# Performance work log

Measured on AMD Instinct MI355X. Metric: run time of the kernel, lower is better.

The kernel has to match this reference:

```python
import jax, jax.numpy as jnp
import numpy as np

NS = 50000   # number of source cells
NT = 50000   # number of target cells
E = 1_600_000  # nnz of neighborhood (avg degree 32)
DIN = 64
DOUT = 64


def setup_inputs() -> dict:
    key = jax.random.key(0)
    ks = jax.random.split(key, 14)
    w_scale = ((2.0 / (DIN + DOUT)) ** 0.5) * 1.414  # xavier_uniform-ish std with gain
    a_scale = (1.0 / (3 * DOUT)) ** 0.5
    nrm = lambda k, s, sc: jax.random.normal(k, s, jnp.float32) * sc
    return {
        "x_source": jax.random.normal(ks[0], (NS, DIN), jnp.float32),
        "x_target": jax.random.normal(ks[1], (NT, DIN), jnp.float32),
        "nb_rows": jax.random.randint(ks[2], (E,), 0, NT, jnp.int32),   # target index of each nnz
        "nb_cols": jax.random.randint(ks[3], (E,), 0, NS, jnp.int32),   # source index of each nnz
        "nb_vals": jax.random.uniform(ks[4], (E,), jnp.float32),        # neighborhood values
        "cci_vals": jax.random.uniform(ks[5], (E,), jnp.float32),       # cci values (same pattern)
        "w_s": nrm(ks[6], (DIN, DOUT), w_scale),
        "w_t": nrm(ks[7], (DIN, DOUT), w_scale),
        "w_s_cci": nrm(ks[8], (DIN, DOUT), w_scale),   # shared: ParameterList([p]*2) aliases one param
        "w_t_cci": nrm(ks[9], (DIN, DOUT), w_scale),
        "src_W": nrm(ks[10], (3, 3 * DOUT, DOUT), a_scale),
        "src_b": jnp.zeros((3, DOUT), jnp.float32),
        "tgt_W": nrm(ks[11], (3, 3 * DOUT, DOUT), a_scale),
        "tgt_b": jnp.zeros((3, DOUT), jnp.float32),
    }


def _pna(seg, nbr, vals, m, W, b, n_seg):
    """PNA aggregation over a sparse neighborhood given as an edge list.
    seg: [E] destination segment ids; nbr: [E] neighbor ids into m; vals: [E] edge weights.
    Aggregators: weighted sum, mean (by neighbor count), max; then Linear(3D -> D)."""
    g = m[nbr] * vals[:, None]                                   # [E, D]
    s_sum = jax.ops.segment_sum(g, seg, num_segments=n_seg)      # [n_seg, D]
    cnt = jax.ops.segment_sum(jnp.ones_like(vals), seg, num_segments=n_seg)
    s_mean = s_sum / jnp.maximum(cnt, 1.0)[:, None]
    s_max = jax.ops.segment_max(g, seg, num_segments=n_seg)
    s_max = jnp.where(jnp.isfinite(s_max), s_max, 0.0)           # empty segments -> 0
    return jnp.concatenate([s_sum, s_mean, s_max], axis=-1) @ W + b


def reference(x_source, x_target, nb_rows, nb_cols, nb_vals, cci_vals,
              w_s, w_t, w_s_cci, w_t_cci, src_W, src_b, tgt_W, tgt_b):
    n_s, n_t = x_source.shape[0], x_target.shape[0]
    # dense projections (w_s_cci / w_t_cci are shared between the two cci branches)
    s_msg = x_source @ w_s          # [NS, DOUT]
    s_msg2 = x_source @ w_s_cci     # used for both cci branches
    t_msg = x_target @ w_t          # [NT, DOUT]
    t_msg2 = x_target @ w_t_cci
    had_vals = cci_vals * nb_vals   # sparse hadamard (same pattern)

    # message on source: aggregate target features along transposed neighborhood [NS, NT]
    msg_src = (_pna(nb_cols, nb_rows, nb_vals, t_msg, src_W[0], src_b[0], n_s)
               + _pna(nb_cols, nb_rows, cci_vals, t_msg2, src_W[1], src_b[1], n_s)
               + _pna(nb_cols, nb_rows, had_vals, t_msg2, src_W[2], src_b[2], n_s))
    # message on target: aggregate source features along neighborhood [NT, NS]
    msg_tgt = (_pna(nb_rows, nb_cols, nb_vals, s_msg, tgt_W[0], tgt_b[0], n_t)
               + _pna(nb_rows, nb_cols, cci_vals, s_msg2, tgt_W[1], tgt_b[1], n_t)
               + _pna(nb_rows, nb_cols, had_vals, s_msg2, tgt_W[2], tgt_b[2], n_t))
    # update_func is None -> return raw messages
    return msg_src, msg_tgt
```

## Files before the change

### kernel.cpp

```cpp
#include <hip/hip_runtime.h>
#include <hip/hip_bf16.h>

typedef unsigned int u32;
typedef unsigned short u16;
typedef unsigned long long u64;
typedef __attribute__((ext_vector_type(8))) short short8;
typedef __attribute__((ext_vector_type(4))) float f32x4;

__device__ __forceinline__ u32 f2bf(float f){
  u32 u = __float_as_uint(f);
  return (u + 0x7fffu + ((u >> 16) & 1u)) >> 16;
}
__device__ __forceinline__ float bflo(u32 p){ return __uint_as_float(p << 16); }
__device__ __forceinline__ float bfhi(u32 p){ return __uint_as_float(p & 0xffff0000u); }

__global__ __launch_bounds__(256) void proj_kernel(
    const float* __restrict__ xs, const float* __restrict__ xt,
    const float* __restrict__ w_s, const float* __restrict__ w_t,
    const float* __restrict__ w_s_cci, const float* __restrict__ w_t_cci,
    u32* __restrict__ mS, u32* __restrict__ mT, int ns, int nt)
{
  __shared__ float wa[4096], wb[4096];
  const int dir = blockIdx.y;
  const float* x  = dir ? xt : xs;
  const float* wA = dir ? w_t : w_s;
  const float* wB = dir ? w_t_cci : w_s_cci;
  u32* out = dir ? mT : mS;
  const int n = dir ? nt : ns;
  const int tid = threadIdx.x;
  for (int i = tid; i < 4096; i += 256){ wa[i] = wA[i]; wb[i] = wB[i]; }
  __syncthreads();
  const int wid = tid >> 6, lane = tid & 63;
  const int slice = lane >> 4, ch = lane & 15;
  for (int row = blockIdx.x*4 + wid; row < n; row += gridDim.x*4){
    float xv = x[(size_t)row*64 + lane];
    float accA = 0.f, accB = 0.f;
    #pragma unroll
    for (int k = 0; k < 64; k++){
      float xk = __shfl(xv, k, 64);
      accA = fmaf(xk, wa[k*64 + lane], accA);
      accB = fmaf(xk, wb[k*64 + lane], accB);
    }
    out[((size_t)slice*n + row)*16 + ch] = f2bf(accA) | (f2bf(accB) << 16);
  }
}

__global__ __launch_bounds__(256) void hist_kernel(
  const int* __restrict__ rows, const int* __restrict__ cols,
  int* cntR, int* cntC, int E,
  const float* __restrict__ srcW, const float* __restrict__ tgtW,
  u16* __restrict__ WtS, u16* __restrict__ WtT)
{
  int e = blockIdx.x*256 + threadIdx.x;
  if (e < E){
    atomicAdd(&cntR[rows[e]], 1);
    atomicAdd(&cntC[cols[e]], 1);
  }
  if (e < 576*64){
    int col = e / 576, k = e - col*576;
    WtS[e] = (u16)f2bf(srcW[(size_t)k*64 + col]);
    WtT[e] = (u16)f2bf(tgtW[(size_t)k*64 + col]);
  }
}

__global__ __launch_bounds__(256) void scan_kernel(
  const int* __restrict__ cntC, const int* __restrict__ cntR,
  int* __restrict__ ptrC, int* __restrict__ ptrR,
  int* __restrict__ curC, int* __restrict__ curR,
  u64* __restrict__ state, int ns, int nt)
{
  const int arr = blockIdx.y;
  const int* cnt = arr ? cntR : cntC;
  int* ptr = arr ? ptrR : ptrC;
  int* cur = arr ? curR : curC;
  const int n = arr ? nt : ns;
  const int nb = (n + 1023) >> 10;
  const int b = blockIdx.x;
  if (b >= nb) return;
  u64* st = state + arr*64;

  const int base = b*1024 + threadIdx.x*4;
  int v[4]; int s = 0;
  #pragma unroll
  for (int i = 0; i < 4; i++){ int idx = base+i; v[i] = (idx < n) ? cnt[idx] : 0; s += v[i]; }
  const int lane = threadIdx.x & 63, wid = threadIdx.x >> 6;
  int ps = s;
  #pragma unroll
  for (int d = 1; d < 64; d <<= 1){ int t = __shfl_up(ps, d, 64); if (lane >= d) ps += t; }
  __shared__ int wsum[4];
  __shared__ int bloff;
  if (lane == 63) wsum[wid] = ps;
  __syncthreads();
  int woff = 0;
  for (int w = 0; w < wid; w++) woff += wsum[w];
  if (threadIdx.x == 0){
    int btot = wsum[0] + wsum[1] + wsum[2] + wsum[3];
    u64 flag1 = (b == 0) ? (2ull << 62) : (1ull << 62);
    __hip_atomic_store(&st[b], flag1 | (u64)(u32)btot,
                       __ATOMIC_RELEASE, __HIP_MEMORY_SCOPE_AGENT);
    int run = 0;
    if (b > 0){
      int i = b - 1;
      while (1){
        u64 p = __hip_atomic_load(&st[i], __ATOMIC_ACQUIRE, __HIP_MEMORY_SCOPE_AGENT);
        u64 fl = p >> 62;
        if (fl == 0){ __builtin_amdgcn_s_sleep(1); continue; }
        run += (int)(u32)p;
        if (fl == 2) break;
        i--;
      }
      __hip_atomic_store(&st[b], (2ull << 62) | (u64)(u32)(run + btot),
                         __ATOMIC_RELEASE, __HIP_MEMORY_SCOPE_AGENT);
    }
    bloff = run;
    if (b == nb - 1) ptr[n] = run + btot;
  }
  __syncthreads();
  int ex = bloff + woff + ps - s;
  #pragma unroll
  for (int i = 0; i < 4; i++){
    int idx = base+i;
    if (idx < n){ ptr[idx] = ex; cur[idx] = ex; }
    ex += v[i];
  }
}

__global__ __launch_bounds__(256) void scatter_kernel(
  const int* __restrict__ rows, const int* __restrict__ cols,
  const float* __restrict__ nbv, const float* __restrict__ ccv,
  int* curR, int* curC,
  int* nbrT, float* w0T, float* w1T,
  int* nbrS, float* w0S, float* w1S, int E)
{
  int e = (blockIdx.x*256 + threadIdx.x)*2;
  if (e + 1 < E){
    int r0 = rows[e], r1 = rows[e+1], c0 = cols[e], c1 = cols[e+1];
    float a0 = nbv[e], a1 = nbv[e+1], b0 = ccv[e], b1 = ccv[e+1];
    int pT0 = atomicAdd(&curR[r0], 1);
    int pT1 = atomicAdd(&curR[r1], 1);
    nbrT[pT0] = c0; w0T[pT0] = a0; w1T[pT0] = b0;
    nbrT[pT1] = c1; w0T[pT1] = a1; w1T[pT1] = b1;
    int pS0 = atomicAdd(&curC[c0], 1);
    int pS1 = atomicAdd(&curC[c1], 1);
    nbrS[pS0] = r0; w0S[pS0] = a0; w1S[pS0] = b0;
    nbrS[pS1] = r1; w0S[pS1] = a1; w1S[pS1] = b1;
  } else if (e < E){
    int r = rows[e], c = cols[e];
    float a = nbv[e], b = ccv[e];
    int pT = atomicAdd(&curR[r], 1);
    nbrT[pT] = c; w0T[pT] = a; w1T[pT] = b;
    int pS = atomicAdd(&curC[c], 1);
    nbrS[pS] = r; w0S[pS] = a; w1S[pS] = b;
  }
}

__global__ __launch_bounds__(256) void repack_kernel(
  const int* __restrict__ nbrT, const float* __restrict__ w0T, const float* __restrict__ w1T,
  const int* __restrict__ nbrS, const float* __restrict__ w0S, const float* __restrict__ w1S,
  u64* __restrict__ recT, u64* __restrict__ recS, int E)
{
  int e = blockIdx.x*256 + threadIdx.x;
  if (e < E){
    {
      float a = w0T[e], b = w1T[e];
      recT[e] = (u64)(u16)nbrT[e] | ((u64)f2bf(a) << 16) | ((u64)f2bf(b) << 32)
              | ((u64)f2bf(a*b) << 48);
    }
    {
      float a = w0S[e], b = w1S[e];
      recS[e] = (u64)(u16)nbrS[e] | ((u64)f2bf(a) << 16) | ((u64)f2bf(b) << 32)
              | ((u64)f2bf(a*b) << 48);
    }
  }
}

__global__ __launch_bounds__(256) void agg_kernel(
  const int* __restrict__ ptr, const u64* __restrict__ rec,
  const u32* __restrict__ mtabFull, u16* __restrict__ stats,
  int nseg, int ntab)
{
  const int slice = blockIdx.z;
  const u32* mtab = mtabFull + (size_t)slice*ntab*16;

  const int wid = threadIdx.x >> 6, lane = threadIdx.x & 63;
  const int seg = blockIdx.x*4 + wid;
  if (seg >= nseg) return;
  const int beg = ptr[seg], end = ptr[seg+1];
  const u32 egrp = (u32)(lane >> 4);
  const char* mt = (const char*)mtab + ((lane & 15) << 2);

  float s0=0.f, s1=0.f, s2=0.f;
  float mx0=-INFINITY, mx1=-INFINITY, mx2=-INFINITY;

  const int cnt = end - beg;
  const u32 nq = (u32)(cnt >> 2);
  const u32 r  = (u32)(cnt & 3);
  u32 e = (u32)beg + egrp;

  #define GREC(i)   (rec[(size_t)(u32)(i)])
  #define GFT(p)    (*(const u32*)(mt + (size_t)((((u32)(p) & 0xffffu) << 6))))
  #define CONSUME(p, f) { \
    u32 lo_ = (u32)(p), hi_ = (u32)((p) >> 32); \
    float a_ = bfhi(lo_), b_ = bflo(hi_), ab_ = bfhi(hi_); \
    float tl_ = bflo(f), th_ = bfhi(f); \
    float g0_ = tl_*a_, g1_ = th_*b_, g2_ = th_*ab_; \
    s0 += g0_; s1 += g1_; s2 += g2_; \
    mx0 = fmaxf(mx0, g0_); mx1 = fmaxf(mx1, g1_); mx2 = fmaxf(mx2, g2_); }

  u32 k = 0;
  for (; k + 8 <= nq; k += 8, e += 32){
    u64 p0 = GREC(e),    p1 = GREC(e+4),  p2 = GREC(e+8),  p3 = GREC(e+12);
    u64 p4 = GREC(e+16), p5 = GREC(e+20), p6 = GREC(e+24), p7 = GREC(e+28);
    u32 f0 = GFT(p0), f1 = GFT(p1), f2 = GFT(p2), f3 = GFT(p3);
    u32 f4 = GFT(p4), f5 = GFT(p5), f6 = GFT(p6), f7 = GFT(p7);
    CONSUME(p0, f0); CONSUME(p1, f1); CONSUME(p2, f2); CONSUME(p3, f3);
    CONSUME(p4, f4); CONSUME(p5, f5); CONSUME(p6, f6); CONSUME(p7, f7);
  }
  for (; k + 2 <= nq; k += 2, e += 8){
    u64 p0 = GREC(e), p1 = GREC(e+4);
    u32 f0 = GFT(p0), f1 = GFT(p1);
    CONSUME(p0, f0); CONSUME(p1, f1);
  }
  if (k < nq){
    u64 p = GREC(e);
    u32 f = GFT(p);
    CONSUME(p, f);
  }
  if (egrp < r){
    u64 p = GREC((u32)beg + 4*nq + egrp);
    u32 f = GFT(p);
    CONSUME(p, f);
  }
  #undef GREC
  #undef GFT
  #undef CONSUME

  #pragma unroll
  for (int d = 16; d <= 32; d <<= 1){
    s0 += __shfl_xor(s0, d, 64);
    s1 += __shfl_xor(s1, d, 64);
    s2 += __shfl_xor(s2, d, 64);
    mx0 = fmaxf(mx0, __shfl_xor(mx0, d, 64));
    mx1 = fmaxf(mx1, __shfl_xor(mx1, d, 64));
    mx2 = fmaxf(mx2, __shfl_xor(mx2, d, 64));
  }
  if (cnt == 0){ mx0 = 0.f; mx1 = 0.f; mx2 = 0.f; }

  if (lane < 16){
    size_t base = ((size_t)slice*nseg + seg)*96 + (lane & 15);
    stats[base      ] = (u16)f2bf(s0);
    stats[base + 16 ] = (u16)f2bf(s1);
    stats[base + 32 ] = (u16)f2bf(s2);
    stats[base + 48 ] = (u16)f2bf(mx0);
    stats[base + 64 ] = (u16)f2bf(mx1);
    stats[base + 80 ] = (u16)f2bf(mx2);
  }
}

#define HROW 584

__global__ __launch_bounds__(256) void lin_kernel(
  const u16* __restrict__ statsS, const u16* __restrict__ statsT,
  const int* __restrict__ ptrC, const int* __restrict__ ptrR,
  const u16* __restrict__ WtS, const u16* __restrict__ WtT,
  const float* __restrict__ srcB, const float* __restrict__ tgtB,
  float* __restrict__ outp, int ns, int nt)
{
  __shared__ u16 h[64*HROW];
  __shared__ float invc[64];
  const int dir = blockIdx.y;
  const u16* stats = dir ? statsT : statsS;
  const int* ptr   = dir ? ptrR : ptrC;
  const u16* Wt    = dir ? WtT : WtS;
  const float* Bg  = dir ? tgtB : srcB;
  const int n = dir ? nt : ns;
  float* out = outp + (dir ? (size_t)ns*64 : 0);
  const int tid = threadIdx.x;
  const int wv = tid >> 6, lane = tid & 63;
  const int seg0 = blockIdx.x * 64;
  if (seg0 >= n) return;

  const int bcol = wv*16 + (lane & 15);
  const int krow = (lane >> 4) * 8;
  short8 bfrag[18];
  #pragma unroll
  for (int t = 0; t < 18; t++)
    bfrag[t] = *(const short8*)&Wt[(size_t)bcol*576 + t*32 + krow];

  if (tid < 64){
    int seg = seg0 + tid;
    float c = (seg < n) ? (float)(ptr[seg+1] - ptr[seg]) : 1.f;
    invc[tid] = 1.f / fmaxf(c, 1.f);
  }
  __syncthreads();

  for (int idx = tid; idx < 64*192; idx += 256){
    int s = idx / 192, i = idx - s*192;
    int blk = i >> 5, cp = (i & 31) * 2;
    int seg = seg0 + s;
    u32 v = 0;
    if (seg < n)
      v = *(const u32*)&stats[((size_t)(cp >> 4)*n + seg)*96 + blk*16 + (cp & 15)];
    u32* hrow = (u32*)&h[s*HROW];
    if (blk < 3){
      hrow[(blk*192 + cp) >> 1] = v;
      float ic = invc[s];
      hrow[(blk*192 + 64 + cp) >> 1] = f2bf(bflo(v)*ic) | (f2bf(bfhi(v)*ic) << 16);
    } else {
      hrow[((blk-3)*192 + 128 + cp) >> 1] = v;
    }
  }
  __syncthreads();

  f32x4 acc[4] = {};
  const int arow = lane & 15;
  #pragma unroll
  for (int t = 0; t < 18; t++){
    #pragma unroll
    for (int rb = 0; rb < 4; rb++){
      short8 a = *(const short8*)&h[(rb*16 + arow)*HROW + t*32 + krow];
      acc[rb] = __builtin_amdgcn_mfma_f32_16x16x32_bf16(a, bfrag[t], acc[rb], 0, 0, 0);
    }
  }

  float bv = Bg[bcol] + Bg[64 + bcol] + Bg[128 + bcol];
  #pragma unroll
  for (int rb = 0; rb < 4; rb++){
    #pragma unroll
    for (int r = 0; r < 4; r++){
      int seg = seg0 + rb*16 + (lane >> 4)*4 + r;
      if (seg < n) out[(size_t)seg*64 + bcol] = acc[rb][r] + bv;
    }
  }
}

extern "C" void kernel_launch(void* const* d_in, const int* in_sizes, int n_in,
                              void* d_out, int out_size, void* d_ws, size_t ws_size,
                              hipStream_t stream)
{
  const float* xs   = (const float*)d_in[0];
  const float* xt   = (const float*)d_in[1];
  const int*   rows = (const int*)  d_in[2];
  const int*   cols = (const int*)  d_in[3];
  const float* nbv  = (const float*)d_in[4];
  const float* ccv  = (const float*)d_in[5];
  const float* w_s  = (const float*)d_in[6];
  const float* w_t  = (const float*)d_in[7];
  const float* w_sc = (const float*)d_in[8];
  const float* w_tc = (const float*)d_in[9];
  const float* srcW = (const float*)d_in[10];
  const float* srcB = (const float*)d_in[11];
  const float* tgtW = (const float*)d_in[12];
  const float* tgtB = (const float*)d_in[13];
  const int ns = in_sizes[0] / 64;
  const int nt = in_sizes[1] / 64;
  const int E  = in_sizes[4];

  char* ws = (char*)d_ws;
  size_t off = 0;
  auto alloc = [&](size_t bytes)->char* {
    char* p = ws + off;
    off = (off + bytes + 255) & ~(size_t)255;
    return p;
  };
  u32* mS    = (u32*)alloc((size_t)ns*64*4);
  u32* mT    = (u32*)alloc((size_t)nt*64*4);
  char* zblk = alloc((size_t)(ns+nt)*4 + 1024);
  int* cntC  = (int*)zblk;
  int* cntR  = cntC + ns;
  u64* state = (u64*)(cntC + ns + nt);
  int* ptrC  = (int*)alloc((size_t)(ns+1)*4);
  int* ptrR  = (int*)alloc((size_t)(nt+1)*4);
  int* curC  = (int*)alloc((size_t)ns*4);
  int* curR  = (int*)alloc((size_t)nt*4);
  int*   nbrS = (int*)  alloc((size_t)E*4);
  float* w0S  = (float*)alloc((size_t)E*4);
  float* w1S  = (float*)alloc((size_t)E*4);
  int*   nbrT = (int*)  alloc((size_t)E*4);
  float* w0T  = (float*)alloc((size_t)E*4);
  float* w1T  = (float*)alloc((size_t)E*4);
  u64* recS   = (u64*)alloc((size_t)E*8);
  u64* recT   = (u64*)alloc((size_t)E*8);
  u16* statsS = (u16*)alloc((size_t)ns*384*2);
  u16* statsT = (u16*)alloc((size_t)nt*384*2);
  u16* WtS    = (u16*)alloc((size_t)576*64*2);
  u16* WtT    = (u16*)alloc((size_t)576*64*2);

  const int mseg = (ns > nt ? ns : nt);
  const int nsb = (mseg + 1023) / 1024;

  hipMemsetAsync(zblk, 0, (size_t)(ns+nt)*4 + 1024, stream);
  proj_kernel<<<dim3(128,2), 256, 0, stream>>>(xs,xt,w_s,w_t,w_sc,w_tc,mS,mT,ns,nt);
  hist_kernel<<<(E+255)/256, 256, 0, stream>>>(rows,cols,cntR,cntC,E,
                                               srcW,tgtW,WtS,WtT);
  scan_kernel<<<dim3(nsb,2), 256, 0, stream>>>(cntC,cntR,ptrC,ptrR,curC,curR,
                                               state,ns,nt);
  scatter_kernel<<<(E/2+255)/256, 256, 0, stream>>>(rows,cols,nbv,ccv,curR,curC,
                                                    nbrT,w0T,w1T,nbrS,w0S,w1S,E);
  repack_kernel<<<(E+255)/256, 256, 0, stream>>>(nbrT,w0T,w1T,nbrS,w0S,w1S,
                                                 recT,recS,E);
  agg_kernel<<<dim3((ns+3)/4, 1, 4), 256, 0, stream>>>(ptrC,recS,mT,statsS,ns,nt);
  agg_kernel<<<dim3((nt+3)/4, 1, 4), 256, 0, stream>>>(ptrR,recT,mS,statsT,nt,ns);
  lin_kernel<<<dim3((mseg+63)/64, 2), 256, 0, stream>>>(statsS,statsT,ptrC,ptrR,
                                                        WtS,WtT,srcB,tgtB,
                                                        (float*)d_out,ns,nt);
}
```

Measured before the change: 845.9 us.

## Replace random edge scatter with two-pass coarse bucket partition then local placement

The edge CSR build previously scattered each edge straight to its final slot with global atomics and random writes across six arrays, then repacked the result. The new path first partitions edges into 512 coarse buckets of 128 segments each, using block-local shared histograms and one global atomic per bucket per block. It writes packed 64-bit temporaries, and a second pass places each record within its bucket's narrow range. This is meant to make writes more local and cut global atomic traffic, at the cost of an extra pass over an E-sized temporary buffer. It relies on segment indices fitting in 16 bits and on at most 512 buckets covering ns and nt.

New measurement: 803.0 us. 1.05x faster.

```diff
diff --git a/kernel.cpp b/kernel.cpp
--- a/kernel.cpp
+++ b/kernel.cpp
@@ -6,6 +6,9 @@
 typedef unsigned long long u64;
 typedef __attribute__((ext_vector_type(8))) short short8;
 typedef __attribute__((ext_vector_type(4))) float f32x4;
+
+#define BSHIFT 7
+#define NBUCK  512
 
 __device__ __forceinline__ u32 f2bf(float f){
   u32 u = __float_as_uint(f);
@@ -125,51 +128,83 @@
   }
 }
 
-__global__ __launch_bounds__(256) void scatter_kernel(
+__global__ __launch_bounds__(512) void binit_kernel(
+  const int* __restrict__ ptrC, const int* __restrict__ ptrR,
+  u32* __restrict__ gcurS, u32* __restrict__ gcurT, int ns, int nt)
+{
+  const int b = threadIdx.x;
+  if (blockIdx.x == 0){
+    int idx = b << BSHIFT; if (idx > ns) idx = ns;
+    gcurS[b] = (u32)ptrC[idx];
+  } else {
+    int idx = b << BSHIFT; if (idx > nt) idx = nt;
+    gcurT[b] = (u32)ptrR[idx];
+  }
+}
+
+__global__ __launch_bounds__(256) void part_kernel(
   const int* __restrict__ rows, const int* __restrict__ cols,
   const float* __restrict__ nbv, const float* __restrict__ ccv,
-  int* curR, int* curC,
-  int* nbrT, float* w0T, float* w1T,
-  int* nbrS, float* w0S, float* w1S, int E)
-{
-  int e = (blockIdx.x*256 + threadIdx.x)*2;
-  if (e + 1 < E){
-    int r0 = rows[e], r1 = rows[e+1], c0 = cols[e], c1 = cols[e+1];
-    float a0 = nbv[e], a1 = nbv[e+1], b0 = ccv[e], b1 = ccv[e+1];
-    int pT0 = atomicAdd(&curR[r0], 1);
-    int pT1 = atomicAdd(&curR[r1], 1);
-    nbrT[pT0] = c0; w0T[pT0] = a0; w1T[pT0] = b0;
-    nbrT[pT1] = c1; w0T[pT1] = a1; w1T[pT1] = b1;
-    int pS0 = atomicAdd(&curC[c0], 1);
-    int pS1 = atomicAdd(&curC[c1], 1);
-    nbrS[pS0] = r0; w0S[pS0] = a0; w1S[pS0] = b0;
-    nbrS[pS1] = r1; w0S[pS1] = a1; w1S[pS1] = b1;
-  } else if (e < E){
-    int r = rows[e], c = cols[e];
-    float a = nbv[e], b = ccv[e];
-    int pT = atomicAdd(&curR[r], 1);
-    nbrT[pT] = c; w0T[pT] = a; w1T[pT] = b;
-    int pS = atomicAdd(&curC[c], 1);
-    nbrS[pS] = r; w0S[pS] = a; w1S[pS] = b;
-  }
-}
-
-__global__ __launch_bounds__(256) void repack_kernel(
-  const int* __restrict__ nbrT, const float* __restrict__ w0T, const float* __restrict__ w1T,
-  const int* __restrict__ nbrS, const float* __restrict__ w0S, const float* __restrict__ w1S,
-  u64* __restrict__ recT, u64* __restrict__ recS, int E)
-{
-  int e = blockIdx.x*256 + threadIdx.x;
-  if (e < E){
-    {
-      float a = w0T[e], b = w1T[e];
-      recT[e] = (u64)(u16)nbrT[e] | ((u64)f2bf(a) << 16) | ((u64)f2bf(b) << 32)
-              | ((u64)f2bf(a*b) << 48);
-    }
-    {
-      float a = w0S[e], b = w1S[e];
-      recS[e] = (u64)(u16)nbrS[e] | ((u64)f2bf(a) << 16) | ((u64)f2bf(b) << 32)
-              | ((u64)f2bf(a*b) << 48);
+  u32* __restrict__ gcurT, u32* __restrict__ gcurS,
+  u64* __restrict__ tmpT, u64* __restrict__ tmpS, int E)
+{
+  __shared__ u32 histT[NBUCK], histS[NBUCK];
+  const int tid = threadIdx.x;
+  const int e0 = blockIdx.x * 2048;
+  for (int i = tid; i < NBUCK; i += 256){ histT[i] = 0; histS[i] = 0; }
+  __syncthreads();
+
+  int r[8], c[8]; float a[8], b[8];
+  #pragma unroll
+  for (int i = 0; i < 8; i++){
+    int e = e0 + i*256 + tid;
+    if (e < E){
+      r[i] = rows[e]; c[i] = cols[e]; a[i] = nbv[e]; b[i] = ccv[e];
+      atomicAdd(&histT[r[i] >> BSHIFT], 1);
+      atomicAdd(&histS[c[i] >> BSHIFT], 1);
+    } else r[i] = -1;
+  }
+  __syncthreads();
+  for (int i = tid; i < NBUCK; i += 256){
+    u32 cT = histT[i]; histT[i] = cT ? atomicAdd(&gcurT[i], cT) : 0;
+    u32 cS = histS[i]; histS[i] = cS ? atomicAdd(&gcurS[i], cS) : 0;
+  }
+  __syncthreads();
+  #pragma unroll
+  for (int i = 0; i < 8; i++){
+    if (r[i] >= 0){
+      u32 fa = f2bf(a[i]), fb = f2bf(b[i]);
+      u64 w = ((u64)fa << 32) | ((u64)fb << 48);
+      u32 pT = atomicAdd(&histT[r[i] >> BSHIFT], 1);
+      tmpT[pT] = w | (u32)r[i] | ((u32)c[i] << 16);
+      u32 pS = atomicAdd(&histS[c[i] >> BSHIFT], 1);
+      tmpS[pS] = w | (u32)c[i] | ((u32)r[i] << 16);
+    }
+  }
+}
+
+__global__ __launch_bounds__(256) void place_kernel(
+  const u64* __restrict__ tmpS, const u64* __restrict__ tmpT,
+  int* __restrict__ curC, int* __restrict__ curR,
+  u64* __restrict__ recS, u64* __restrict__ recT, int E)
+{
+  const int dir = blockIdx.y;
+  const u64* tmp = dir ? tmpT : tmpS;
+  int* cur = dir ? curR : curC;
+  u64* rec = dir ? recT : recS;
+  const int base = blockIdx.x*1024 + threadIdx.x;
+  #pragma unroll
+  for (int i = 0; i < 4; i++){
+    int e = base + i*256;
+    if (e < E){
+      u64 t = tmp[e];
+      u32 lo = (u32)t;
+      int seg = (int)(lo & 0xffffu);
+      u32 fa = (u32)(t >> 32) & 0xffffu, fb = (u32)(t >> 48);
+      float fab = __uint_as_float(fa << 16) * __uint_as_float(fb << 16);
+      int p = atomicAdd(&cur[seg], 1);
+      rec[p] = (u64)(lo >> 16) | ((u64)fa << 16) | ((u64)fb << 32)
+             | ((u64)f2bf(fab) << 48);
     }
   }
 }
@@ -373,14 +408,12 @@
   int* ptrR  = (int*)alloc((size_t)(nt+1)*4);
   int* curC  = (int*)alloc((size_t)ns*4);
   int* curR  = (int*)alloc((size_t)nt*4);
-  int*   nbrS = (int*)  alloc((size_t)E*4);
-  float* w0S  = (float*)alloc((size_t)E*4);
-  float* w1S  = (float*)alloc((size_t)E*4);
-  int*   nbrT = (int*)  alloc((size_t)E*4);
-  float* w0T  = (float*)alloc((size_t)E*4);
-  float* w1T  = (float*)alloc((size_t)E*4);
-  u64* recS   = (u64*)alloc((size_t)E*8);
-  u64* recT   = (u64*)alloc((size_t)E*8);
+  u32* gcurS = (u32*)alloc((size_t)NBUCK*4);
+  u32* gcurT = (u32*)alloc((size_t)NBUCK*4);
+  u64* tmpS  = (u64*)alloc((size_t)E*8);
+  u64* tmpT  = (u64*)alloc((size_t)E*8);
+  u64* recS  = (u64*)alloc((size_t)E*8);
+  u64* recT  = (u64*)alloc((size_t)E*8);
   u16* statsS = (u16*)alloc((size_t)ns*384*2);
   u16* statsT = (u16*)alloc((size_t)nt*384*2);
   u16* WtS    = (u16*)alloc((size_t)576*64*2);
@@ -395,10 +428,11 @@
                                                srcW,tgtW,WtS,WtT);
   scan_kernel<<<dim3(nsb,2), 256, 0, stream>>>(cntC,cntR,ptrC,ptrR,curC,curR,
                                                state,ns,nt);
-  scatter_kernel<<<(E/2+255)/256, 256, 0, stream>>>(rows,cols,nbv,ccv,curR,curC,
-                                                    nbrT,w0T,w1T,nbrS,w0S,w1S,E);
-  repack_kernel<<<(E+255)/256, 256, 0, stream>>>(nbrT,w0T,w1T,nbrS,w0S,w1S,
-                                                 recT,recS,E);
+  binit_kernel<<<2, NBUCK, 0, stream>>>(ptrC,ptrR,gcurS,gcurT,ns,nt);
+  part_kernel<<<(E+2047)/2048, 256, 0, stream>>>(rows,cols,nbv,ccv,
+                                                 gcurT,gcurS,tmpT,tmpS,E);
+  place_kernel<<<dim3((E+1023)/1024, 2), 256, 0, stream>>>(tmpS,tmpT,curC,curR,
+                                                           recS,recT,E);
   agg_kernel<<<dim3((ns+3)/4, 1, 4), 256, 0, stream>>>(ptrC,recS,mT,statsS,ns,nt);
   agg_kernel<<<dim3((nt+3)/4, 1, 4), 256, 0, stream>>>(ptrR,recT,mS,statsT,nt,ns);
   lin_kernel<<<dim3((mseg+63)/64, 2), 256, 0, stream>>>(statsS,statsT,ptrC,ptrR,
```
